# Kernel optimization log

Measured on AMD Instinct MI355X. Metric: run time of the kernel, lower is better.

## Reference

```python
import jax, jax.numpy as jnp
import numpy as np

B, T, I, H, O = 1024, 512, 128, 256, 64


def setup_inputs() -> dict:
    key = jax.random.key(0)
    ks = jax.random.split(key, 12)
    def lin(k, shape, fan_in):
        return jax.random.uniform(k, shape, jnp.float32, -1.0, 1.0) / np.sqrt(fan_in)
    return {
        "x": jax.random.normal(ks[0], (B, T, I), jnp.float32),
        "h0": jnp.zeros((B, H), jnp.float32),
        # GRUCell params (gate order: r, z, n as in PyTorch)
        "W_ih": lin(ks[1], (3 * H, I), H),
        "b_ih": lin(ks[2], (3 * H,), H),
        "W_hh": lin(ks[3], (3 * H, H), H),
        "b_hh": lin(ks[4], (3 * H,), H),
        # input_transform Linear(I -> H)
        "Wt": lin(ks[5], (H, I), I),
        "bt": lin(ks[6], (H,), I),
        # output_proj Linear(H -> O)
        "Wo": lin(ks[7], (O, H), H),
        "bo": lin(ks[8], (O,), H),
        # gate_proj Linear(H -> O)
        "Wg": lin(ks[9], (O, H), H),
        "bg": lin(ks[10], (O,), H),
    }


def reference(x, h0, W_ih, b_ih, W_hh, b_hh, Wt, bt, Wo, bo, Wg, bg):
    # Precompute all input-side projections with big GEMMs (time-major for scan)
    xi = jnp.einsum("bti,gi->tbg", x, W_ih) + b_ih          # [T,B,3H]
    ti = jax.nn.silu(jnp.einsum("bti,hi->tbh", x, Wt) + bt)  # [T,B,H]

    def step(h, inp):
        xi_t, ti_t = inp
        hh = h @ W_hh.T + b_hh                               # [B,3H]
        xr, xz, xn = jnp.split(xi_t, 3, axis=-1)
        hr, hz, hn = jnp.split(hh, 3, axis=-1)
        r = jax.nn.sigmoid(xr + hr)
        z = jax.nn.sigmoid(xz + hz)
        n = jnp.tanh(xn + r * hn)
        h_new = (1.0 - z) * n + z * h
        proj = (h_new + ti_t) @ Wo.T + bo                    # [B,O]
        gate = jax.nn.sigmoid(h_new @ Wg.T + bg)             # [B,O]
        return h_new, proj * gate

    _, outs = jax.lax.scan(step, h0, (xi, ti))               # outs: [T,B,O]
    return jnp.mean(outs, axis=0)                            # [B,O]
```

## Files before the change

### kernel.cpp

```cpp
#include <hip/hip_runtime.h>
#include <hip/hip_bf16.h>


typedef __attribute__((ext_vector_type(8))) __bf16 bf16x8;
typedef __attribute__((ext_vector_type(4))) __bf16 bf16x4;
typedef __attribute__((ext_vector_type(2))) __bf16 bf16x2;
typedef __attribute__((ext_vector_type(4))) float f32x4;

#define MFMA(a, b, c) __builtin_amdgcn_mfma_f32_16x16x32_bf16(a, b, c, 0, 0, 0)

__device__ __forceinline__ float fsig(float v) {
  float e = __builtin_amdgcn_exp2f(v * -1.442695041f);
  return __builtin_amdgcn_rcpf(1.0f + e);
}
__device__ __forceinline__ float ftanh(float v) {
  float e = __builtin_amdgcn_exp2f(v * 2.885390082f);
  return 1.0f - 2.0f * __builtin_amdgcn_rcpf(1.0f + e);
}

#define O_WIN 0u
#define O_WHH 262144u
#define O_WO  655360u
#define O_WG  688128u
#define O_B1  720896u
#define O_H   724992u
#define O_ACC 1773568u
#define O_TIO 2035712u

__global__ void k1_prep(const float* __restrict__ Wih, const float* __restrict__ Wt,
                        const float* __restrict__ Whh, const float* __restrict__ Wo,
                        const float* __restrict__ Wg, const float* __restrict__ bih,
                        const float* __restrict__ bhh, const float* __restrict__ bt,
                        const float* __restrict__ h0, char* __restrict__ ws) {
  unsigned n = blockIdx.x * 256u + threadIdx.x;
  __bf16* win = (__bf16*)(ws + O_WIN);
  __bf16* whh = (__bf16*)(ws + O_WHH);
  __bf16* wo = (__bf16*)(ws + O_WO);
  __bf16* wg = (__bf16*)(ws + O_WG);
  float* b1 = (float*)(ws + O_B1);
  float* hb = (float*)(ws + O_H);
  float* ac = (float*)(ws + O_ACC);
  if (n < 98304u) win[n] = (__bf16)Wih[n];
  else if (n < 131072u) { unsigned i = n - 98304u; win[98304u + i] = (__bf16)Wt[i]; }
  else if (n < 327680u) { unsigned i = n - 131072u; whh[i] = (__bf16)Whh[i]; }
  else if (n < 344064u) { unsigned i = n - 327680u; wo[i] = (__bf16)Wo[i]; }
  else if (n < 360448u) { unsigned i = n - 344064u; wg[i] = (__bf16)Wg[i]; }
  else if (n < 361472u) {
    unsigned i = n - 360448u;
    float v = (i < 512u) ? (bih[i] + bhh[i]) : ((i < 768u) ? bih[i] : bt[i - 768u]);
    b1[i] = v;
  } else if (n < 623616u) { unsigned i = n - 361472u; hb[i] = h0[i]; }
  else if (n < 689152u) { unsigned i = n - 623616u; ac[i] = 0.0f; }
}

__global__ __launch_bounds__(256, 2) void k2_xi(
    const float* __restrict__ x, const __bf16* __restrict__ win,
    const float* __restrict__ b1, __bf16* __restrict__ xi, int t0, int tcbits) {
  extern __shared__ char sm2[];
  __bf16* Asm = (__bf16*)sm2;
  __bf16* Bsm = (__bf16*)(sm2 + 34816);
  const int tid = threadIdx.x;
  const int lane = tid & 63, wv = tid >> 6;
  const int m0 = blockIdx.x * 128;
  const int tcm = (1 << tcbits) - 1;
#pragma unroll
  for (int rnd = 0; rnd < 16; ++rnd) {
    int row = rnd * 8 + (tid >> 5);
    int cr = m0 + row;
    int bb = cr >> tcbits, tt = cr & tcm;
    const float* xr = x + ((size_t)bb * 512 + (size_t)(t0 + tt)) * 128 + (tid & 31) * 4;
    float4 v = *(const float4*)xr;
    bf16x4 b4 = {(__bf16)v.x, (__bf16)v.y, (__bf16)v.z, (__bf16)v.w};
    *(bf16x4*)&Asm[row * 136 + (tid & 31) * 4] = b4;
  }
  for (int nc = 0; nc < 6; ++nc) {
    __syncthreads();
#pragma unroll
    for (int rnd = 0; rnd < 8; ++rnd) {
      int rr = rnd * 16 + (tid >> 4);
      uint4 w4 = *(const uint4*)(win + (size_t)(nc * 128 + rr) * 128 + (tid & 15) * 8);
      *(uint4*)&Bsm[rr * 136 + (tid & 15) * 8] = w4;
    }
    __syncthreads();
    f32x4 zv = {0.f, 0.f, 0.f, 0.f};
    f32x4 acc[2][8];
#pragma unroll
    for (int mi = 0; mi < 2; ++mi)
#pragma unroll
      for (int nt = 0; nt < 8; ++nt) acc[mi][nt] = zv;
#pragma unroll
    for (int kt = 0; kt < 4; ++kt) {
      bf16x8 a0 = *(const bf16x8*)&Asm[(wv * 32 + (lane & 15)) * 136 + kt * 32 + (lane >> 4) * 8];
      bf16x8 a1 = *(const bf16x8*)&Asm[(wv * 32 + 16 + (lane & 15)) * 136 + kt * 32 + (lane >> 4) * 8];
#pragma unroll
      for (int nt = 0; nt < 8; ++nt) {
        bf16x8 b = *(const bf16x8*)&Bsm[(nt * 16 + (lane & 15)) * 136 + kt * 32 + (lane >> 4) * 8];
        acc[0][nt] = MFMA(a0, b, acc[0][nt]);
        acc[1][nt] = MFMA(a1, b, acc[1][nt]);
      }
    }
    __syncthreads();
#pragma unroll
    for (int nt = 0; nt < 8; ++nt) {
      float bv = b1[nc * 128 + nt * 16 + (lane & 15)];
#pragma unroll
      for (int mi = 0; mi < 2; ++mi)
#pragma unroll
        for (int r = 0; r < 4; ++r) {
          int rowb = wv * 32 + mi * 16 + (lane >> 4) * 4 + r;
          Bsm[rowb * 136 + nt * 16 + (lane & 15)] = (__bf16)(acc[mi][nt][r] + bv);
        }
    }
    __syncthreads();
#pragma unroll
    for (int rnd = 0; rnd < 8; ++rnd) {
      int row = rnd * 16 + (tid >> 4);
      int cr = m0 + row;
      int bb = cr >> tcbits, tt = cr & tcm;
      uint4 v = *(const uint4*)&Bsm[row * 136 + (tid & 15) * 8];
      *(uint4*)(xi + ((size_t)tt * 1024 + bb) * 768 + nc * 128 + (tid & 15) * 8) = v;
    }
  }
}

__global__ __launch_bounds__(256, 1) void k2_tio(
    const float* __restrict__ x, const __bf16* __restrict__ win,
    const __bf16* __restrict__ wo, const float* __restrict__ b1,
    const float* __restrict__ bo, __bf16* __restrict__ tio, int t0, int tcbits) {
  extern __shared__ char sm3[];
  __bf16* Asm = (__bf16*)sm3;
  __bf16* Bsm = (__bf16*)(sm3 + 34816);
  __bf16* Ti = (__bf16*)(sm3 + 69632);
  const int tid = threadIdx.x;
  const int lane = tid & 63, wv = tid >> 6;
  const int m0 = blockIdx.x * 128;
  const int tcm = (1 << tcbits) - 1;
#pragma unroll
  for (int rnd = 0; rnd < 16; ++rnd) {
    int row = rnd * 8 + (tid >> 5);
    int cr = m0 + row;
    int bb = cr >> tcbits, tt = cr & tcm;
    const float* xr = x + ((size_t)bb * 512 + (size_t)(t0 + tt)) * 128 + (tid & 31) * 4;
    float4 v = *(const float4*)xr;
    bf16x4 b4 = {(__bf16)v.x, (__bf16)v.y, (__bf16)v.z, (__bf16)v.w};
    *(bf16x4*)&Asm[row * 136 + (tid & 31) * 4] = b4;
  }
  for (int nc = 0; nc < 2; ++nc) {
    __syncthreads();
#pragma unroll
    for (int rnd = 0; rnd < 8; ++rnd) {
      int rr = rnd * 16 + (tid >> 4);
      uint4 w4 = *(const uint4*)(win + (size_t)(98304 / 128 + nc * 128 + rr) * 128 + (tid & 15) * 8);
      *(uint4*)&Bsm[rr * 136 + (tid & 15) * 8] = w4;
    }
    __syncthreads();
    f32x4 zv = {0.f, 0.f, 0.f, 0.f};
    f32x4 acc[2][8];
#pragma unroll
    for (int mi = 0; mi < 2; ++mi)
#pragma unroll
      for (int nt = 0; nt < 8; ++nt) acc[mi][nt] = zv;
#pragma unroll
    for (int kt = 0; kt < 4; ++kt) {
      bf16x8 a0 = *(const bf16x8*)&Asm[(wv * 32 + (lane & 15)) * 136 + kt * 32 + (lane >> 4) * 8];
      bf16x8 a1 = *(const bf16x8*)&Asm[(wv * 32 + 16 + (lane & 15)) * 136 + kt * 32 + (lane >> 4) * 8];
#pragma unroll
      for (int nt = 0; nt < 8; ++nt) {
        bf16x8 b = *(const bf16x8*)&Bsm[(nt * 16 + (lane & 15)) * 136 + kt * 32 + (lane >> 4) * 8];
        acc[0][nt] = MFMA(a0, b, acc[0][nt]);
        acc[1][nt] = MFMA(a1, b, acc[1][nt]);
      }
    }
#pragma unroll
    for (int nt = 0; nt < 8; ++nt) {
      float bv = b1[768 + nc * 128 + nt * 16 + (lane & 15)];
#pragma unroll
      for (int mi = 0; mi < 2; ++mi)
#pragma unroll
        for (int r = 0; r < 4; ++r) {
          int rowb = wv * 32 + mi * 16 + (lane >> 4) * 4 + r;
          float s = acc[mi][nt][r] + bv;
          s = s * __builtin_amdgcn_rcpf(1.0f + __builtin_amdgcn_exp2f(s * -1.442695041f));
          Ti[rowb * 264 + nc * 128 + nt * 16 + (lane & 15)] = (__bf16)s;
        }
    }
  }
  __syncthreads();
  for (int i = tid; i < 2048; i += 256) {
    int row = i >> 5;
    int c8 = (i & 31) * 8;
    *(uint4*)&Bsm[row * 264 + c8] = *(const uint4*)(wo + row * 256 + c8);
  }
  __syncthreads();
  f32x4 zv = {0.f, 0.f, 0.f, 0.f};
  f32x4 acc2[2][4];
#pragma unroll
  for (int mi = 0; mi < 2; ++mi)
#pragma unroll
    for (int nt = 0; nt < 4; ++nt) acc2[mi][nt] = zv;
#pragma unroll
  for (int kt = 0; kt < 8; ++kt) {
    bf16x8 a0 = *(const bf16x8*)&Ti[(wv * 32 + (lane & 15)) * 264 + kt * 32 + (lane >> 4) * 8];
    bf16x8 a1 = *(const bf16x8*)&Ti[(wv * 32 + 16 + (lane & 15)) * 264 + kt * 32 + (lane >> 4) * 8];
#pragma unroll
    for (int nt = 0; nt < 4; ++nt) {
      bf16x8 b = *(const bf16x8*)&Bsm[(nt * 16 + (lane & 15)) * 264 + kt * 32 + (lane >> 4) * 8];
      acc2[0][nt] = MFMA(a0, b, acc2[0][nt]);
      acc2[1][nt] = MFMA(a1, b, acc2[1][nt]);
    }
  }
#pragma unroll
  for (int nt = 0; nt < 4; ++nt) {
    int col = nt * 16 + (lane & 15);
    float bv = bo[col];
#pragma unroll
    for (int mi = 0; mi < 2; ++mi)
#pragma unroll
      for (int r = 0; r < 4; ++r) {
        int rowb = wv * 32 + mi * 16 + (lane >> 4) * 4 + r;
        int cr = m0 + rowb;
        int bb = cr >> tcbits, tt = cr & tcm;
        tio[((size_t)tt * 1024 + bb) * 64 + col] = (__bf16)(acc2[mi][nt][r] + bv);
      }
  }
}

__global__ __launch_bounds__(256, 1) void k3_rec(
    const __bf16* __restrict__ xi, const __bf16* __restrict__ tio,
    const __bf16* __restrict__ whh, const __bf16* __restrict__ wo,
    const __bf16* __restrict__ wg, const float* __restrict__ bhn,
    const float* __restrict__ bg, float* __restrict__ hbuf,
    float* __restrict__ accb, int TC) {
  extern __shared__ char sm[];
  __bf16* hbase = (__bf16*)sm;
  float* preb = (float*)(sm + 16896);
  __bf16* xib = (__bf16*)(sm + 29952);
  __bf16* wow = (__bf16*)(sm + 43264);
  const int tid = threadIdx.x;
  const int lane = tid & 63, wv = tid >> 6;
  const int b0 = blockIdx.x * 4;
  const int l15 = lane & 15, lg = lane >> 4;
  float* pre_w = preb + wv * 816;

  bf16x8 wf[4][3][8];
#pragma unroll
  for (int p = 0; p < 4; ++p)
#pragma unroll
    for (int g = 0; g < 3; ++g)
#pragma unroll
      for (int kt = 0; kt < 8; ++kt) {
        int rowg = g * 256 + wv * 64 + p * 16 + l15;
        wf[p][g][kt] = *(const bf16x8*)(whh + (size_t)rowg * 256 + kt * 32 + lg * 8);
      }
  for (int i = tid; i < 4096; i += 256) {
    int row = i >> 5;
    int c8 = (i & 31) * 8;
    const __bf16* srcw = (row < 64) ? (wo + row * 256 + c8) : (wg + (row - 64) * 256 + c8);
    *(uint4*)&wow[row * 264 + c8] = *(const uint4*)srcw;
  }
  for (int i = tid; i < 4224; i += 256) ((unsigned*)sm)[i] = 0u;
  __syncthreads();
  const int row = lg;
  const int c4 = l15 * 4;
  float hreg[4];
  {
    f32x4 h4 = *(const f32x4*)(hbuf + (size_t)(b0 + row) * 256 + wv * 64 + c4);
    hreg[0] = h4[0]; hreg[1] = h4[1]; hreg[2] = h4[2]; hreg[3] = h4[3];
    bf16x4 hb = {(__bf16)h4[0], (__bf16)h4[1], (__bf16)h4[2], (__bf16)h4[3]};
    *(bf16x4*)&hbase[row * 264 + wv * 64 + c4] = hb;
  }
  float bhnp[4];
#pragma unroll
  for (int p = 0; p < 4; ++p) bhnp[p] = bhn[wv * 64 + p * 16 + l15];
  const float bgv = bg[wv * 16 + l15];
  float oacc[4] = {0.f, 0.f, 0.f, 0.f};
  if (lane < 16) {
#pragma unroll
    for (int r = 0; r < 4; ++r) oacc[r] = accb[(size_t)(b0 + r) * 64 + wv * 16 + lane];
  }
  {
    const uint2* s0 = (const uint2*)(xi + (size_t)b0 * 768);
    uint2* d0 = (uint2*)xib;
    d0[tid] = s0[tid]; d0[tid + 256] = s0[tid + 256]; d0[tid + 512] = s0[tid + 512];
    if (tid < 64) ((uint2*)(xib + 3072))[tid] = ((const uint2*)(tio + (size_t)b0 * 64))[tid];
  }
  float tioR[4] = {0.f, 0.f, 0.f, 0.f};
  __syncthreads();

#pragma unroll 1
  for (int t = 0; t < TC; ++t) {
    const int cur = t & 1, nxt = cur ^ 1;
    const __bf16* hcur = hbase + cur * 4224;
    __bf16* hnxt = hbase + nxt * 4224;
    const __bf16* xc = xib + cur * 3328;
    int tn = (t + 1 < TC) ? (t + 1) : t;
    uint2 pf0, pf1, pf2, pft;
    {
      const uint2* s = (const uint2*)(xi + ((size_t)tn * 1024 + b0) * 768);
      pf0 = s[tid]; pf1 = s[tid + 256]; pf2 = s[tid + 512];
      if (tid < 64) pft = ((const uint2*)(tio + ((size_t)tn * 1024 + b0) * 64))[tid];
    }
    bf16x8 afr[8];
#pragma unroll
    for (int kt = 0; kt < 8; ++kt)
      afr[kt] = *(const bf16x8*)&hcur[l15 * 264 + kt * 32 + lg * 8];
#pragma unroll
    for (int p = 0; p < 4; ++p) {
      f32x4 ar = {0.f, 0.f, 0.f, 0.f}, az = {0.f, 0.f, 0.f, 0.f};
      f32x4 an = {bhnp[p], bhnp[p], bhnp[p], bhnp[p]};
#pragma unroll
      for (int kt = 0; kt < 8; ++kt) {
        ar = MFMA(afr[kt], wf[p][0][kt], ar);
        az = MFMA(afr[kt], wf[p][1][kt], az);
        an = MFMA(afr[kt], wf[p][2][kt], an);
      }
      if (lane < 16) {
#pragma unroll
        for (int r = 0; r < 4; ++r) {
          pre_w[r * 68 + p * 16 + lane] = ar[r];
          pre_w[272 + r * 68 + p * 16 + lane] = az[r];
          pre_w[544 + r * 68 + p * 16 + lane] = an[r];
        }
      }
    }
    {
      f32x4 hr = *(const f32x4*)&pre_w[row * 68 + c4];
      f32x4 hz = *(const f32x4*)&pre_w[272 + row * 68 + c4];
      f32x4 hn = *(const f32x4*)&pre_w[544 + row * 68 + c4];
      bf16x4 xr4 = *(const bf16x4*)&xc[row * 768 + wv * 64 + c4];
      bf16x4 xz4 = *(const bf16x4*)&xc[row * 768 + 256 + wv * 64 + c4];
      bf16x4 xn4 = *(const bf16x4*)&xc[row * 768 + 512 + wv * 64 + c4];
#pragma unroll
      for (int j = 0; j < 4; ++j) {
        float r_ = fsig((float)xr4[j] + hr[j]);
        float z_ = fsig((float)xz4[j] + hz[j]);
        float n_ = ftanh((float)xn4[j] + r_ * hn[j]);
        hreg[j] = n_ + z_ * (hreg[j] - n_);
      }
      bf16x4 hb = {(__bf16)hreg[0], (__bf16)hreg[1], (__bf16)hreg[2], (__bf16)hreg[3]};
      *(bf16x4*)&hnxt[row * 264 + wv * 64 + c4] = hb;
    }
    {
      f32x4 po = {0.f, 0.f, 0.f, 0.f};
      f32x4 pg = {bgv, bgv, bgv, bgv};
#pragma unroll
      for (int kt = 0; kt < 8; ++kt) {
        bf16x8 bfo = *(const bf16x8*)&wow[(wv * 16 + l15) * 264 + kt * 32 + lg * 8];
        bf16x8 bfg = *(const bf16x8*)&wow[(64 + wv * 16 + l15) * 264 + kt * 32 + lg * 8];
        po = MFMA(afr[kt], bfo, po);
        pg = MFMA(afr[kt], bfg, pg);
      }
      if (t >= 1 && lane < 16) {
#pragma unroll
        for (int r = 0; r < 4; ++r)
          oacc[r] += (po[r] + tioR[r]) * fsig(pg[r]);
      }
    }
    if (lane < 16) {
#pragma unroll
      for (int r = 0; r < 4; ++r) tioR[r] = (float)xc[3072 + r * 64 + wv * 16 + lane];
    }
    {
      uint2* d = (uint2*)(xib + nxt * 3328);
      d[tid] = pf0; d[tid + 256] = pf1; d[tid + 512] = pf2;
      if (tid < 64) ((uint2*)(xib + nxt * 3328 + 3072))[tid] = pft;
    }
    __syncthreads();
  }
  {
    const __bf16* hcur = hbase + (TC & 1) * 4224;
    bf16x8 af[8];
#pragma unroll
    for (int kt = 0; kt < 8; ++kt)
      af[kt] = *(const bf16x8*)&hcur[l15 * 264 + kt * 32 + lg * 8];
    f32x4 po = {0.f, 0.f, 0.f, 0.f};
    f32x4 pg = {bgv, bgv, bgv, bgv};
#pragma unroll
    for (int kt = 0; kt < 8; ++kt) {
      bf16x8 bfo = *(const bf16x8*)&wow[(wv * 16 + l15) * 264 + kt * 32 + lg * 8];
      bf16x8 bfg = *(const bf16x8*)&wow[(64 + wv * 16 + l15) * 264 + kt * 32 + lg * 8];
      po = MFMA(af[kt], bfo, po);
      pg = MFMA(af[kt], bfg, pg);
    }
    if (lane < 16) {
#pragma unroll
      for (int r = 0; r < 4; ++r)
        oacc[r] += (po[r] + tioR[r]) * fsig(pg[r]);
    }
  }
  {
    f32x4 h4 = {hreg[0], hreg[1], hreg[2], hreg[3]};
    *(f32x4*)(hbuf + (size_t)(b0 + row) * 256 + wv * 64 + c4) = h4;
  }
  if (lane < 16) {
#pragma unroll
    for (int r = 0; r < 4; ++r) accb[(size_t)(b0 + r) * 64 + wv * 16 + lane] = oacc[r];
  }
}

__global__ void k4_out(const float* __restrict__ accb, float* __restrict__ out) {
  int i = blockIdx.x * 256 + threadIdx.x;
  out[i] = accb[i] * (1.0f / 512.0f);
}

extern "C" void kernel_launch(void* const* d_in, const int* in_sizes, int n_in,
                              void* d_out, int out_size, void* d_ws, size_t ws_size,
                              hipStream_t stream) {
  const float* x = (const float*)d_in[0];
  const float* h0 = (const float*)d_in[1];
  const float* Wih = (const float*)d_in[2];
  const float* bih = (const float*)d_in[3];
  const float* Whh = (const float*)d_in[4];
  const float* bhh = (const float*)d_in[5];
  const float* Wt = (const float*)d_in[6];
  const float* bt = (const float*)d_in[7];
  const float* Wo = (const float*)d_in[8];
  const float* bo = (const float*)d_in[9];
  const float* Wg = (const float*)d_in[10];
  const float* bg = (const float*)d_in[11];
  float* out = (float*)d_out;
  char* ws = (char*)d_ws;

  int TC = 512;
  while (TC > 1 && (2035712ull + (size_t)TC * 1703936ull) > ws_size) TC >>= 1;
  int tcbits = 0;
  while ((1 << tcbits) != TC) ++tcbits;

  __bf16* win = (__bf16*)(ws + O_WIN);
  __bf16* whhb = (__bf16*)(ws + O_WHH);
  __bf16* wob = (__bf16*)(ws + O_WO);
  __bf16* wgb = (__bf16*)(ws + O_WG);
  float* b1 = (float*)(ws + O_B1);
  float* hbuf = (float*)(ws + O_H);
  float* accb = (float*)(ws + O_ACC);
  __bf16* tioc = (__bf16*)(ws + O_TIO);
  __bf16* xic = (__bf16*)(ws + O_TIO + (size_t)TC * 131072u);

  (void)hipFuncSetAttribute((const void*)k2_xi, hipFuncAttributeMaxDynamicSharedMemorySize, 69632);
  (void)hipFuncSetAttribute((const void*)k2_tio, hipFuncAttributeMaxDynamicSharedMemorySize, 137216);
  (void)hipFuncSetAttribute((const void*)k3_rec, hipFuncAttributeMaxDynamicSharedMemorySize, 110848);

  k1_prep<<<2692, 256, 0, stream>>>(Wih, Wt, Whh, Wo, Wg, bih, bhh, bt, h0, ws);
  int nch = 512 / TC;
  for (int c = 0; c < nch; ++c) {
    int t0 = c * TC;
    k2_xi<<<8 * TC, 256, 69632, stream>>>(x, win, b1, xic, t0, tcbits);
    k2_tio<<<8 * TC, 256, 137216, stream>>>(x, win, wob, b1, bo, tioc, t0, tcbits);
    k3_rec<<<256, 256, 110848, stream>>>(xic, tioc, whhb, wob, wgb, bhh + 512, bg, hbuf, accb, TC);
  }
  k4_out<<<256, 256, 0, stream>>>(accb, out);
}
```

Before: 2.159 ms.

## Keep output/gate weights in registers and prefetch xi via direct global-to-LDS loads

```diff
diff --git a/kernel.cpp b/kernel.cpp
--- a/kernel.cpp
+++ b/kernel.cpp
@@ -16,6 +16,11 @@
 __device__ __forceinline__ float ftanh(float v) {
   float e = __builtin_amdgcn_exp2f(v * 2.885390082f);
   return 1.0f - 2.0f * __builtin_amdgcn_rcpf(1.0f + e);
+}
+__device__ __forceinline__ void gload16(const void* g, void* l) {
+  __builtin_amdgcn_global_load_lds(
+      (const __attribute__((address_space(1))) unsigned*)g,
+      (__attribute__((address_space(3))) unsigned*)l, 16, 0, 0);
 }
 
 #define O_WIN 0u
@@ -235,7 +240,6 @@
   __bf16* hbase = (__bf16*)sm;
   float* preb = (float*)(sm + 16896);
   __bf16* xib = (__bf16*)(sm + 29952);
-  __bf16* wow = (__bf16*)(sm + 43264);
   const int tid = threadIdx.x;
   const int lane = tid & 63, wv = tid >> 6;
   const int b0 = blockIdx.x * 4;
@@ -252,11 +256,11 @@
         int rowg = g * 256 + wv * 64 + p * 16 + l15;
         wf[p][g][kt] = *(const bf16x8*)(whh + (size_t)rowg * 256 + kt * 32 + lg * 8);
       }
-  for (int i = tid; i < 4096; i += 256) {
-    int row = i >> 5;
-    int c8 = (i & 31) * 8;
-    const __bf16* srcw = (row < 64) ? (wo + row * 256 + c8) : (wg + (row - 64) * 256 + c8);
-    *(uint4*)&wow[row * 264 + c8] = *(const uint4*)srcw;
+  bf16x8 wpo[8], wpg[8];
+#pragma unroll
+  for (int kt = 0; kt < 8; ++kt) {
+    wpo[kt] = *(const bf16x8*)(wo + (size_t)(wv * 16 + l15) * 256 + kt * 32 + lg * 8);
+    wpg[kt] = *(const bf16x8*)(wg + (size_t)(wv * 16 + l15) * 256 + kt * 32 + lg * 8);
   }
   for (int i = tid; i < 4224; i += 256) ((unsigned*)sm)[i] = 0u;
   __syncthreads();
@@ -279,10 +283,12 @@
     for (int r = 0; r < 4; ++r) oacc[r] = accb[(size_t)(b0 + r) * 64 + wv * 16 + lane];
   }
   {
-    const uint2* s0 = (const uint2*)(xi + (size_t)b0 * 768);
-    uint2* d0 = (uint2*)xib;
-    d0[tid] = s0[tid]; d0[tid + 256] = s0[tid + 256]; d0[tid + 512] = s0[tid + 512];
-    if (tid < 64) ((uint2*)(xib + 3072))[tid] = ((const uint2*)(tio + (size_t)b0 * 64))[tid];
+    const char* xs = (const char*)(xi + (size_t)b0 * 768);
+    const char* ts = (const char*)(tio + (size_t)b0 * 64);
+    char* xd = (char*)xib;
+    gload16(xs + wv * 1024 + lane * 16, xd + wv * 1024);
+    if (wv < 2) gload16(xs + 4096 + wv * 1024 + lane * 16, xd + 4096 + wv * 1024);
+    if (wv == 2) gload16(ts + lane * 16, xd + 6144);
   }
   float tioR[4] = {0.f, 0.f, 0.f, 0.f};
   __syncthreads();
@@ -292,13 +298,15 @@
     const int cur = t & 1, nxt = cur ^ 1;
     const __bf16* hcur = hbase + cur * 4224;
     __bf16* hnxt = hbase + nxt * 4224;
-    const __bf16* xc = xib + cur * 3328;
+    const __bf16* xc = xib + cur * 3584;
     int tn = (t + 1 < TC) ? (t + 1) : t;
-    uint2 pf0, pf1, pf2, pft;
     {
-      const uint2* s = (const uint2*)(xi + ((size_t)tn * 1024 + b0) * 768);
-      pf0 = s[tid]; pf1 = s[tid + 256]; pf2 = s[tid + 512];
-      if (tid < 64) pft = ((const uint2*)(tio + ((size_t)tn * 1024 + b0) * 64))[tid];
+      const char* xs = (const char*)(xi + ((size_t)tn * 1024 + b0) * 768);
+      const char* ts = (const char*)(tio + ((size_t)tn * 1024 + b0) * 64);
+      char* xd = (char*)(xib + nxt * 3584);
+      gload16(xs + wv * 1024 + lane * 16, xd + wv * 1024);
+      if (wv < 2) gload16(xs + 4096 + wv * 1024 + lane * 16, xd + 4096 + wv * 1024);
+      if (wv == 2) gload16(ts + lane * 16, xd + 6144);
     }
     bf16x8 afr[8];
 #pragma unroll
@@ -322,6 +330,13 @@
           pre_w[544 + r * 68 + p * 16 + lane] = an[r];
         }
       }
+    }
+    f32x4 po = {0.f, 0.f, 0.f, 0.f};
+    f32x4 pg = {bgv, bgv, bgv, bgv};
+#pragma unroll
+    for (int kt = 0; kt < 8; ++kt) {
+      po = MFMA(afr[kt], wpo[kt], po);
+      pg = MFMA(afr[kt], wpg[kt], pg);
     }
     {
       f32x4 hr = *(const f32x4*)&pre_w[row * 68 + c4];
@@ -340,30 +355,14 @@
       bf16x4 hb = {(__bf16)hreg[0], (__bf16)hreg[1], (__bf16)hreg[2], (__bf16)hreg[3]};
       *(bf16x4*)&hnxt[row * 264 + wv * 64 + c4] = hb;
     }
-    {
-      f32x4 po = {0.f, 0.f, 0.f, 0.f};
-      f32x4 pg = {bgv, bgv, bgv, bgv};
-#pragma unroll
-      for (int kt = 0; kt < 8; ++kt) {
-        bf16x8 bfo = *(const bf16x8*)&wow[(wv * 16 + l15) * 264 + kt * 32 + lg * 8];
-        bf16x8 bfg = *(const bf16x8*)&wow[(64 + wv * 16 + l15) * 264 + kt * 32 + lg * 8];
-        po = MFMA(afr[kt], bfo, po);
-        pg = MFMA(afr[kt], bfg, pg);
-      }
-      if (t >= 1 && lane < 16) {
-#pragma unroll
-        for (int r = 0; r < 4; ++r)
-          oacc[r] += (po[r] + tioR[r]) * fsig(pg[r]);
-      }
+    if (t >= 1 && lane < 16) {
+#pragma unroll
+      for (int r = 0; r < 4; ++r)
+        oacc[r] += (po[r] + tioR[r]) * fsig(pg[r]);
     }
     if (lane < 16) {
 #pragma unroll
       for (int r = 0; r < 4; ++r) tioR[r] = (float)xc[3072 + r * 64 + wv * 16 + lane];
-    }
-    {
-      uint2* d = (uint2*)(xib + nxt * 3328);
-      d[tid] = pf0; d[tid + 256] = pf1; d[tid + 512] = pf2;
-      if (tid < 64) ((uint2*)(xib + nxt * 3328 + 3072))[tid] = pft;
     }
     __syncthreads();
   }
@@ -377,10 +376,8 @@
     f32x4 pg = {bgv, bgv, bgv, bgv};
 #pragma unroll
     for (int kt = 0; kt < 8; ++kt) {
-      bf16x8 bfo = *(const bf16x8*)&wow[(wv * 16 + l15) * 264 + kt * 32 + lg * 8];
-      bf16x8 bfg = *(const bf16x8*)&wow[(64 + wv * 16 + l15) * 264 + kt * 32 + lg * 8];
-      po = MFMA(af[kt], bfo, po);
-      pg = MFMA(af[kt], bfg, pg);
+      po = MFMA(af[kt], wpo[kt], po);
+      pg = MFMA(af[kt], wpg[kt], pg);
     }
     if (lane < 16) {
 #pragma unroll
@@ -438,7 +435,7 @@
 
   (void)hipFuncSetAttribute((const void*)k2_xi, hipFuncAttributeMaxDynamicSharedMemorySize, 69632);
   (void)hipFuncSetAttribute((const void*)k2_tio, hipFuncAttributeMaxDynamicSharedMemorySize, 137216);
-  (void)hipFuncSetAttribute((const void*)k3_rec, hipFuncAttributeMaxDynamicSharedMemorySize, 110848);
+  (void)hipFuncSetAttribute((const void*)k3_rec, hipFuncAttributeMaxDynamicSharedMemorySize, 44288);
 
   k1_prep<<<2692, 256, 0, stream>>>(Wih, Wt, Whh, Wo, Wg, bih, bhh, bt, h0, ws);
   int nch = 512 / TC;
@@ -446,7 +443,7 @@
     int t0 = c * TC;
     k2_xi<<<8 * TC, 256, 69632, stream>>>(x, win, b1, xic, t0, tcbits);
     k2_tio<<<8 * TC, 256, 137216, stream>>>(x, win, wob, b1, bo, tioc, t0, tcbits);
-    k3_rec<<<256, 256, 110848, stream>>>(xic, tioc, whhb, wob, wgb, bhh + 512, bg, hbuf, accb, TC);
+    k3_rec<<<256, 256, 44288, stream>>>(xic, tioc, whhb, wob, wgb, bhh + 512, bg, hbuf, accb, TC);
   }
   k4_out<<<256, 256, 0, stream>>>(accb, out);
 }
```

Measured after the change: 2.887 ms. 33.7% more time.
